# Performance work log

Hardware: AMD Instinct MI355X
Metric: run time of the kernel (lower is better)

## Reference

```python
import jax, jax.numpy as jnp
import numpy as np

N = 20000      # nodes
E = 320000     # edges (before self-loops)
D = 128        # esm_embeds
H = 4          # n_heads (layer 1)
G = 256        # graphs in batch
SLOPE = 0.2    # GATConv default negative_slope


def setup_inputs() -> dict:
    key = jax.random.key(0)
    ks = jax.random.split(key, 16)
    x = jax.random.normal(ks[0], (N, D), jnp.float32)
    src = jax.random.randint(ks[1], (E,), 0, N)
    off = jax.random.randint(ks[2], (E,), 1, N)
    dst = (src + off) % N  # guaranteed no self-loops (PyG removes then re-adds them)
    edge_index = jnp.stack([src, dst]).astype(jnp.int64)
    batch = jnp.sort(jax.random.randint(ks[3], (N,), 0, G)).astype(jnp.int64)
    s = 0.05
    W1 = jax.random.normal(ks[4], (D, H * D), jnp.float32) * s
    a_src1 = jax.random.normal(ks[5], (1, H, D), jnp.float32) * s
    a_dst1 = jax.random.normal(ks[6], (1, H, D), jnp.float32) * s
    b1 = jnp.zeros((H * D,), jnp.float32)
    W2 = jax.random.normal(ks[7], (H * D, D), jnp.float32) * s
    a_src2 = jax.random.normal(ks[8], (1, 1, D), jnp.float32) * s
    a_dst2 = jax.random.normal(ks[9], (1, 1, D), jnp.float32) * s
    b2 = jnp.zeros((D,), jnp.float32)
    fc1_w = jax.random.normal(ks[10], (D, 16), jnp.float32) * s
    fc1_b = jnp.zeros((16,), jnp.float32)
    fc2_w = jax.random.normal(ks[11], (16, 1), jnp.float32) * s
    fc2_b = jnp.zeros((1,), jnp.float32)
    return {"x": x, "edge_index": edge_index, "batch": batch,
            "W1": W1, "a_src1": a_src1, "a_dst1": a_dst1, "b1": b1,
            "W2": W2, "a_src2": a_src2, "a_dst2": a_dst2, "b2": b2,
            "fc1_w": fc1_w, "fc1_b": fc1_b, "fc2_w": fc2_w, "fc2_b": fc2_b}


def _gat_conv(h, src, dst, a_src, a_dst, n):
    """h: [n, heads, C]; returns aggregated [n, heads, C] (PyG GATConv message passing)."""
    al_s = jnp.sum(h * a_src, axis=-1)  # [n, heads]
    al_d = jnp.sum(h * a_dst, axis=-1)  # [n, heads]
    e = jax.nn.leaky_relu(al_s[src] + al_d[dst], SLOPE)  # [Etot, heads]
    m = jax.lax.stop_gradient(jax.ops.segment_max(e, dst, num_segments=n))
    ex = jnp.exp(e - m[dst])
    denom = jax.ops.segment_sum(ex, dst, num_segments=n)
    alpha = ex / denom[dst]                               # per-destination softmax
    msg = h[src] * alpha[..., None]                       # [Etot, heads, C]
    return jax.ops.segment_sum(msg, dst, num_segments=n)


def reference(x, edge_index, batch, W1, a_src1, a_dst1, b1,
              W2, a_src2, a_dst2, b2, fc1_w, fc1_b, fc2_w, fc2_b):
    n = x.shape[0]
    loop = jnp.arange(n, dtype=edge_index.dtype)
    src = jnp.concatenate([edge_index[0], loop])  # GATConv add_self_loops=True
    dst = jnp.concatenate([edge_index[1], loop])
    # layer 1: heads=H, concat -> [n, H*D], then ELU (dropout is identity in eval)
    h1 = (x @ W1).reshape(n, H, D)
    o1 = _gat_conv(h1, src, dst, a_src1, a_dst1, n).reshape(n, H * D) + b1
    x1 = jax.nn.elu(o1)
    # layer 2: heads=1, concat -> [n, D], then ReLU
    h2 = (x1 @ W2).reshape(n, 1, D)
    o2 = _gat_conv(h2, src, dst, a_src2, a_dst2, n).reshape(n, D) + b2
    x2 = jax.nn.relu(o2)
    # global max pool over graphs; x2 >= 0 so clamping handles any empty segment
    pooled = jnp.maximum(jax.ops.segment_max(x2, batch, num_segments=G), 0.0)
    hfc = jax.nn.relu(pooled @ fc1_w + fc1_b)
    return hfc @ fc2_w + fc2_b  # [G, 1]
```

## Files before the change

kernel.cpp:

```cpp
#include <hip/hip_runtime.h>
#include <hip/hip_fp16.h>

#define N_NODES 20000
#define E_EDGES 320000
#define D_DIM   128
#define H1HEADS 4
#define G_GRAPHS 256
#define SLOPE   0.2f

typedef _Float16 h8 __attribute__((ext_vector_type(8)));
typedef float float4v __attribute__((ext_vector_type(4)));

__global__ void cntprep_k(const int* __restrict__ dst, int* __restrict__ cnt,
                          const float* __restrict__ W1, __half* __restrict__ w1t,
                          const float* __restrict__ W2, __half* __restrict__ w2t) {
    int i = blockIdx.x * blockDim.x + threadIdx.x;
    if (i < E_EDGES) atomicAdd(&cnt[dst[i]], 1);
    if (i < 128 * 512) {
        {
            int k = i >> 9, n = i & 511;
            w1t[n * 128 + k] = __float2half(W1[i]);
        }
        {
            int k = i >> 7, n = i & 127;
            w2t[n * 512 + k] = __float2half(W2[i]);
        }
    }
}

#define SCAN_B 79
__global__ __launch_bounds__(256) void scan1_k(const int* __restrict__ cnt,
                                               int* __restrict__ part) {
    __shared__ int s[256];
    int t = threadIdx.x;
    int i = blockIdx.x * 256 + t;
    int v = (i < N_NODES) ? cnt[i] : 0;
    s[t] = v;
    __syncthreads();
    for (int off = 128; off > 0; off >>= 1) {
        if (t < off) s[t] += s[t + off];
        __syncthreads();
    }
    if (t == 0) part[blockIdx.x] = s[0];
}
__global__ __launch_bounds__(128) void scan2_k(int* __restrict__ part) {
    __shared__ int s[128];
    int t = threadIdx.x;
    int v = (t < SCAN_B) ? part[t] : 0;
    s[t] = v;
    __syncthreads();
    for (int off = 1; off < 128; off <<= 1) {
        int u = (t >= off) ? s[t - off] : 0;
        __syncthreads();
        s[t] += u;
        __syncthreads();
    }
    if (t < SCAN_B) part[t] = s[t] - v;
}
__global__ __launch_bounds__(256) void scan3_k(const int* __restrict__ cnt,
                                               const int* __restrict__ part,
                                               int* __restrict__ rowptr) {
    __shared__ int s[256];
    int t = threadIdx.x;
    int i = blockIdx.x * 256 + t;
    int v = (i < N_NODES) ? cnt[i] : 0;
    s[t] = v;
    __syncthreads();
    for (int off = 1; off < 256; off <<= 1) {
        int u = (t >= off) ? s[t - off] : 0;
        __syncthreads();
        s[t] += u;
        __syncthreads();
    }
    if (i < N_NODES) rowptr[i] = part[blockIdx.x] + s[t] - v;
    if (blockIdx.x == 0 && t == 0) rowptr[N_NODES] = E_EDGES;
}

__global__ void scat_k(const int* __restrict__ src, const int* __restrict__ dst,
                       const int* __restrict__ rowptr, int* __restrict__ cur,
                       int* __restrict__ csrsrc) {
    int e = blockIdx.x * blockDim.x + threadIdx.x;
    if (e >= E_EDGES) return;
    int d = dst[e];
    int p = rowptr[d] + atomicAdd(&cur[d], 1);
    csrsrc[p] = src[e];
}

__device__ __forceinline__ int bitonic64(int key, int lane) {
#pragma unroll
    for (int k = 2; k <= 64; k <<= 1) {
#pragma unroll
        for (int j = k >> 1; j > 0; j >>= 1) {
            int other = __shfl_xor(key, j);
            bool up = ((lane & k) == 0);
            bool lower = ((lane & j) == 0);
            int mn = min(key, other), mx = max(key, other);
            key = (up == lower) ? mn : mx;
        }
    }
    return key;
}

__global__ __launch_bounds__(256) void sortb_k(const int* __restrict__ rowptr,
                                               int* __restrict__ csrsrc) {
    const int node = (blockIdx.x * blockDim.x + threadIdx.x) >> 6;
    if (node >= N_NODES) return;
    const int lane = threadIdx.x & 63;
    const int r0 = rowptr[node];
    const int deg = rowptr[node + 1] - r0;
    if (deg <= 1 || deg > 64) return;
    int key = 0x7FFFFFFF;
    if (lane < deg) key = csrsrc[r0 + lane];
    key = bitonic64(key, lane);
    if (lane < deg) csrsrc[r0 + lane] = key;
}

__device__ __forceinline__ void store_val(__half* p, float v) { *p = __float2half(v); }
__device__ __forceinline__ void store_val(float* p, float v) { *p = v; }

template <typename OT>
__global__ __launch_bounds__(256) void fgemm_k(const float* __restrict__ A,
                                               const __half* __restrict__ BT,
                                               const int M, const int N, const int K,
                                               OT* __restrict__ C,
                                               float* __restrict__ als,
                                               float* __restrict__ ald,
                                               const float* __restrict__ asrc,
                                               const float* __restrict__ adst) {
    constexpr int SA = 72;
    __shared__ __half Ah[64 * SA], Al[64 * SA];
    __shared__ float sdot[64][2][2];
    const int t = threadIdx.x;
    const int wave = t >> 6, lane = t & 63;
    const int q = lane >> 4, rr = lane & 15;
    const int row0 = blockIdx.x * 64;
    const int col0 = blockIdx.y * 128;
    const int wm = wave & 1, wn = wave >> 1;
    const int H = gridDim.y;

    float4v acc[2][4];
#pragma unroll
    for (int i = 0; i < 2; ++i)
#pragma unroll
        for (int j = 0; j < 4; ++j) acc[i][j] = (float4v){0.f, 0.f, 0.f, 0.f};

    for (int kc = 0; kc < K; kc += 64) {
        __syncthreads();
#pragma unroll
        for (int i = 0; i < 4; ++i) {
            int u = t + i * 256;
            int m = u >> 4, mac = u & 15;
            int r = row0 + m;
            float4 fv = make_float4(0.f, 0.f, 0.f, 0.f);
            if (r < M) fv = *(const float4*)(A + (size_t)r * K + kc + mac * 4);
            union { __half h[4]; uint2 u2; } ph, pl;
            float f[4] = {fv.x, fv.y, fv.z, fv.w};
#pragma unroll
            for (int k = 0; k < 4; ++k) {
                __half hb = __float2half(f[k]);
                ph.h[k] = hb;
                pl.h[k] = __float2half(f[k] - __half2float(hb));
            }
            *(uint2*)(Ah + m * SA + mac * 4) = ph.u2;
            *(uint2*)(Al + m * SA + mac * 4) = pl.u2;
        }
        __syncthreads();
#pragma unroll
        for (int ks = 0; ks < 2; ++ks) {
            const int ko = ks * 32 + q * 8;
            h8 ah[2], alo[2], bh[4];
#pragma unroll
            for (int mt = 0; mt < 2; ++mt) {
                int m = (wm * 2 + mt) * 16 + rr;
                ah[mt]  = *(const h8*)(Ah + m * SA + ko);
                alo[mt] = *(const h8*)(Al + m * SA + ko);
            }
#pragma unroll
            for (int nt = 0; nt < 4; ++nt) {
                int n = (wn * 4 + nt) * 16 + rr;
                bh[nt] = *(const h8*)(BT + (size_t)(col0 + n) * K + kc + ko);
            }
#pragma unroll
            for (int mt = 0; mt < 2; ++mt)
#pragma unroll
                for (int nt = 0; nt < 4; ++nt) {
                    acc[mt][nt] = __builtin_amdgcn_mfma_f32_16x16x32_f16(
                        ah[mt], bh[nt], acc[mt][nt], 0, 0, 0);
                    acc[mt][nt] = __builtin_amdgcn_mfma_f32_16x16x32_f16(
                        alo[mt], bh[nt], acc[mt][nt], 0, 0, 0);
                }
        }
    }
#pragma unroll
    for (int mt = 0; mt < 2; ++mt) {
#pragma unroll
        for (int reg = 0; reg < 4; ++reg) {
            int r = row0 + (wm * 2 + mt) * 16 + q * 4 + reg;
            if (r < M) {
#pragma unroll
                for (int nt = 0; nt < 4; ++nt) {
                    int c = col0 + (wn * 4 + nt) * 16 + rr;
                    store_val(&C[(size_t)r * N + c], acc[mt][nt][reg]);
                }
            }
        }
    }
    ((float*)sdot)[t] = 0.f;
    __syncthreads();
    const float* as = asrc + blockIdx.y * 128;
    const float* ad = adst + blockIdx.y * 128;
#pragma unroll
    for (int mt = 0; mt < 2; ++mt) {
#pragma unroll
        for (int reg = 0; reg < 4; ++reg) {
            float ps = 0.f, pd = 0.f;
#pragma unroll
            for (int nt = 0; nt < 4; ++nt) {
                int cc = (wn * 4 + nt) * 16 + rr;
                float v = acc[mt][nt][reg];
                ps += v * as[cc];
                pd += v * ad[cc];
            }
#pragma unroll
            for (int off = 1; off < 16; off <<= 1) {
                ps += __shfl_xor(ps, off);
                pd += __shfl_xor(pd, off);
            }
            if (rr == 0) {
                int row = (wm * 2 + mt) * 16 + q * 4 + reg;
                sdot[row][wn][0] = ps;
                sdot[row][wn][1] = pd;
            }
        }
    }
    __syncthreads();
    if (t < 64) {
        int r = row0 + t;
        if (r < M) {
            als[r * H + blockIdx.y] = sdot[t][0][0] + sdot[t][1][0];
            ald[r * H + blockIdx.y] = sdot[t][0][1] + sdot[t][1][1];
        }
    }
}

__device__ __forceinline__ float lrelu(float v) { return (v > 0.f) ? v : SLOPE * v; }

__global__ __launch_bounds__(64) void agg1_k(const __half* __restrict__ h,
                                             const float4* __restrict__ als4,
                                             const float4* __restrict__ ald4,
                                             const int* __restrict__ rowptr,
                                             const int* __restrict__ csrsrc,
                                             const float* __restrict__ bias,
                                             float* __restrict__ x1) {
    __shared__ int   ss[64];
    __shared__ float ws[64][4];
    const int node = blockIdx.x;
    const int lane = threadIdx.x;
    const int head = lane >> 4;
    const int r0 = rowptr[node];
    const int deg = rowptr[node + 1] - r0;
    const int tot = deg + 1;
    const float4 aldn = ald4[node];

    float acc[8] = {};
    float4 d4;

    if (tot <= 64) {
        int s = node;
        if (lane < deg) s = csrsrc[r0 + lane];
        float4 l4 = make_float4(-1e30f, -1e30f, -1e30f, -1e30f);
        if (lane < tot) {
            float4 a = als4[s];
            l4.x = lrelu(a.x + aldn.x); l4.y = lrelu(a.y + aldn.y);
            l4.z = lrelu(a.z + aldn.z); l4.w = lrelu(a.w + aldn.w);
        }
        float4 m4 = l4;
#pragma unroll
        for (int off = 32; off > 0; off >>= 1) {
            m4.x = fmaxf(m4.x, __shfl_xor(m4.x, off));
            m4.y = fmaxf(m4.y, __shfl_xor(m4.y, off));
            m4.z = fmaxf(m4.z, __shfl_xor(m4.z, off));
            m4.w = fmaxf(m4.w, __shfl_xor(m4.w, off));
        }
        float4 w4 = make_float4(0.f, 0.f, 0.f, 0.f);
        if (lane < tot) {
            w4.x = expf(l4.x - m4.x); w4.y = expf(l4.y - m4.y);
            w4.z = expf(l4.z - m4.z); w4.w = expf(l4.w - m4.w);
        }
        d4 = w4;
#pragma unroll
        for (int off = 32; off > 0; off >>= 1) {
            d4.x += __shfl_xor(d4.x, off);
            d4.y += __shfl_xor(d4.y, off);
            d4.z += __shfl_xor(d4.z, off);
            d4.w += __shfl_xor(d4.w, off);
        }
        ss[lane] = s;
        *(float4*)&ws[lane][0] = w4;
        const uint4* hp = (const uint4*)h;
        int j = 0;
        for (; j + 8 <= tot; j += 8) {
            uint4 k0 = hp[(size_t)ss[j]     * 64 + lane];
            uint4 k1 = hp[(size_t)ss[j + 1] * 64 + lane];
            uint4 k2 = hp[(size_t)ss[j + 2] * 64 + lane];
            uint4 k3 = hp[(size_t)ss[j + 3] * 64 + lane];
            uint4 k4 = hp[(size_t)ss[j + 4] * 64 + lane];
            uint4 k5 = hp[(size_t)ss[j + 5] * 64 + lane];
            uint4 k6 = hp[(size_t)ss[j + 6] * 64 + lane];
            uint4 k7 = hp[(size_t)ss[j + 7] * 64 + lane];
            float w0 = ws[j][head],     w1 = ws[j + 1][head];
            float w2 = ws[j + 2][head], w3 = ws[j + 3][head];
            float w4s = ws[j + 4][head], w5 = ws[j + 5][head];
            float w6 = ws[j + 6][head], w7 = ws[j + 7][head];
            const __half *p0 = (const __half*)&k0, *p1 = (const __half*)&k1;
            const __half *p2 = (const __half*)&k2, *p3 = (const __half*)&k3;
            const __half *p4 = (const __half*)&k4, *p5 = (const __half*)&k5;
            const __half *p6 = (const __half*)&k6, *p7 = (const __half*)&k7;
#pragma unroll
            for (int k = 0; k < 8; ++k) acc[k] += w0 * __half2float(p0[k]);
#pragma unroll
            for (int k = 0; k < 8; ++k) acc[k] += w1 * __half2float(p1[k]);
#pragma unroll
            for (int k = 0; k < 8; ++k) acc[k] += w2 * __half2float(p2[k]);
#pragma unroll
            for (int k = 0; k < 8; ++k) acc[k] += w3 * __half2float(p3[k]);
#pragma unroll
            for (int k = 0; k < 8; ++k) acc[k] += w4s * __half2float(p4[k]);
#pragma unroll
            for (int k = 0; k < 8; ++k) acc[k] += w5 * __half2float(p5[k]);
#pragma unroll
            for (int k = 0; k < 8; ++k) acc[k] += w6 * __half2float(p6[k]);
#pragma unroll
            for (int k = 0; k < 8; ++k) acc[k] += w7 * __half2float(p7[k]);
        }
        for (; j + 4 <= tot; j += 4) {
            uint4 k0 = hp[(size_t)ss[j]     * 64 + lane];
            uint4 k1 = hp[(size_t)ss[j + 1] * 64 + lane];
            uint4 k2 = hp[(size_t)ss[j + 2] * 64 + lane];
            uint4 k3 = hp[(size_t)ss[j + 3] * 64 + lane];
            float w0 = ws[j][head],     w1 = ws[j + 1][head];
            float w2 = ws[j + 2][head], w3 = ws[j + 3][head];
            const __half *p0 = (const __half*)&k0, *p1 = (const __half*)&k1;
            const __half *p2 = (const __half*)&k2, *p3 = (const __half*)&k3;
#pragma unroll
            for (int k = 0; k < 8; ++k) acc[k] += w0 * __half2float(p0[k]);
#pragma unroll
            for (int k = 0; k < 8; ++k) acc[k] += w1 * __half2float(p1[k]);
#pragma unroll
            for (int k = 0; k < 8; ++k) acc[k] += w2 * __half2float(p2[k]);
#pragma unroll
            for (int k = 0; k < 8; ++k) acc[k] += w3 * __half2float(p3[k]);
        }
        for (; j < tot; ++j) {
            uint4 pk = hp[(size_t)ss[j] * 64 + lane];
            float wj = ws[j][head];
            const __half* p = (const __half*)&pk;
#pragma unroll
            for (int k = 0; k < 8; ++k) acc[k] += wj * __half2float(p[k]);
        }
    } else {
        float4 m4 = make_float4(-1e30f, -1e30f, -1e30f, -1e30f);
        for (int base = 0; base < tot; base += 64) {
            int j = base + lane;
            float4 l4 = make_float4(-1e30f, -1e30f, -1e30f, -1e30f);
            if (j < tot) {
                int s = (j < deg) ? csrsrc[r0 + j] : node;
                float4 a = als4[s];
                l4.x = lrelu(a.x + aldn.x); l4.y = lrelu(a.y + aldn.y);
                l4.z = lrelu(a.z + aldn.z); l4.w = lrelu(a.w + aldn.w);
            }
#pragma unroll
            for (int off = 32; off > 0; off >>= 1) {
                l4.x = fmaxf(l4.x, __shfl_xor(l4.x, off));
                l4.y = fmaxf(l4.y, __shfl_xor(l4.y, off));
                l4.z = fmaxf(l4.z, __shfl_xor(l4.z, off));
                l4.w = fmaxf(l4.w, __shfl_xor(l4.w, off));
            }
            m4.x = fmaxf(m4.x, l4.x); m4.y = fmaxf(m4.y, l4.y);
            m4.z = fmaxf(m4.z, l4.z); m4.w = fmaxf(m4.w, l4.w);
        }
        d4 = make_float4(0.f, 0.f, 0.f, 0.f);
        for (int base = 0; base < tot; base += 64) {
            int j = base + lane;
            int s = node;
            float4 w4 = make_float4(0.f, 0.f, 0.f, 0.f);
            if (j < tot) {
                if (j < deg) s = csrsrc[r0 + j];
                float4 a = als4[s];
                w4.x = expf(lrelu(a.x + aldn.x) - m4.x);
                w4.y = expf(lrelu(a.y + aldn.y) - m4.y);
                w4.z = expf(lrelu(a.z + aldn.z) - m4.z);
                w4.w = expf(lrelu(a.w + aldn.w) - m4.w);
            }
            float4 p4 = w4;
#pragma unroll
            for (int off = 32; off > 0; off >>= 1) {
                p4.x += __shfl_xor(p4.x, off);
                p4.y += __shfl_xor(p4.y, off);
                p4.z += __shfl_xor(p4.z, off);
                p4.w += __shfl_xor(p4.w, off);
            }
            d4.x += p4.x; d4.y += p4.y; d4.z += p4.z; d4.w += p4.w;
            int lim = min(64, tot - base);
            for (int j2 = 0; j2 < lim; ++j2) {
                int sj = __shfl(s, j2);
                float w0 = __shfl(w4.x, j2), w1 = __shfl(w4.y, j2);
                float w2 = __shfl(w4.z, j2), w3 = __shfl(w4.w, j2);
                float wj = (head < 2) ? (head == 0 ? w0 : w1) : (head == 2 ? w2 : w3);
                const uint4 pk = *((const uint4*)(h + (size_t)sj * 512) + lane);
                const __half* p = (const __half*)&pk;
#pragma unroll
                for (int k = 0; k < 8; ++k) acc[k] += wj * __half2float(p[k]);
            }
        }
    }

    const float dsel = (head < 2) ? (head == 0 ? d4.x : d4.y) : (head == 2 ? d4.z : d4.w);
    const float inv = 1.f / dsel;
    const float4 b0 = ((const float4*)bias)[lane * 2];
    const float4 b1 = ((const float4*)bias)[lane * 2 + 1];
    float v[8];
    v[0] = acc[0] * inv + b0.x; v[1] = acc[1] * inv + b0.y;
    v[2] = acc[2] * inv + b0.z; v[3] = acc[3] * inv + b0.w;
    v[4] = acc[4] * inv + b1.x; v[5] = acc[5] * inv + b1.y;
    v[6] = acc[6] * inv + b1.z; v[7] = acc[7] * inv + b1.w;
#pragma unroll
    for (int k = 0; k < 8; ++k) v[k] = (v[k] > 0.f) ? v[k] : expm1f(v[k]);
    float4* orow = (float4*)(x1 + (size_t)node * 512);
    orow[lane * 2]     = make_float4(v[0], v[1], v[2], v[3]);
    orow[lane * 2 + 1] = make_float4(v[4], v[5], v[6], v[7]);
}

__global__ __launch_bounds__(64) void agg2_k(const __half* __restrict__ h,
                                             const float* __restrict__ als,
                                             const float* __restrict__ ald,
                                             const int* __restrict__ rowptr,
                                             const int* __restrict__ csrsrc,
                                             const float* __restrict__ bias,
                                             const int* __restrict__ batch,
                                             int* __restrict__ pooled) {
    __shared__ int   ss[64];
    __shared__ float ws[64];
    const int node = blockIdx.x;
    const int lane = threadIdx.x;
    const int r0 = rowptr[node];
    const int deg = rowptr[node + 1] - r0;
    const int tot = deg + 1;
    const float aldn = ald[node];

    float acc0 = 0.f, acc1 = 0.f;
    float denom;

    if (tot <= 64) {
        int s = node;
        if (lane < deg) s = csrsrc[r0 + lane];
        float l = -1e30f, w = 0.f;
        if (lane < tot) l = lrelu(als[s] + aldn);
        float m = l;
#pragma unroll
        for (int off = 32; off > 0; off >>= 1) m = fmaxf(m, __shfl_xor(m, off));
        if (lane < tot) w = expf(l - m);
        denom = w;
#pragma unroll
        for (int off = 32; off > 0; off >>= 1) denom += __shfl_xor(denom, off);
        ss[lane] = s;
        ws[lane] = w;
        const unsigned* hp = (const unsigned*)h;
        int j = 0;
        for (; j + 8 <= tot; j += 8) {
            unsigned k0 = hp[(size_t)ss[j]     * 64 + lane];
            unsigned k1 = hp[(size_t)ss[j + 1] * 64 + lane];
            unsigned k2 = hp[(size_t)ss[j + 2] * 64 + lane];
            unsigned k3 = hp[(size_t)ss[j + 3] * 64 + lane];
            unsigned k4 = hp[(size_t)ss[j + 4] * 64 + lane];
            unsigned k5 = hp[(size_t)ss[j + 5] * 64 + lane];
            unsigned k6 = hp[(size_t)ss[j + 6] * 64 + lane];
            unsigned k7 = hp[(size_t)ss[j + 7] * 64 + lane];
            float w0 = ws[j], w1 = ws[j + 1], w2 = ws[j + 2], w3 = ws[j + 3];
            float w4 = ws[j + 4], w5 = ws[j + 5], w6 = ws[j + 6], w7 = ws[j + 7];
            float2 f0 = __half22float2(*(__half2*)&k0);
            float2 f1 = __half22float2(*(__half2*)&k1);
            float2 f2 = __half22float2(*(__half2*)&k2);
            float2 f3 = __half22float2(*(__half2*)&k3);
            float2 f4 = __half22float2(*(__half2*)&k4);
            float2 f5 = __half22float2(*(__half2*)&k5);
            float2 f6 = __half22float2(*(__half2*)&k6);
            float2 f7 = __half22float2(*(__half2*)&k7);
            acc0 += w0 * f0.x; acc1 += w0 * f0.y;
            acc0 += w1 * f1.x; acc1 += w1 * f1.y;
            acc0 += w2 * f2.x; acc1 += w2 * f2.y;
            acc0 += w3 * f3.x; acc1 += w3 * f3.y;
            acc0 += w4 * f4.x; acc1 += w4 * f4.y;
            acc0 += w5 * f5.x; acc1 += w5 * f5.y;
            acc0 += w6 * f6.x; acc1 += w6 * f6.y;
            acc0 += w7 * f7.x; acc1 += w7 * f7.y;
        }
        for (; j < tot; ++j) {
            unsigned pk = hp[(size_t)ss[j] * 64 + lane];
            float wj = ws[j];
            float2 f = __half22float2(*(__half2*)&pk);
            acc0 += wj * f.x;
            acc1 += wj * f.y;
        }
    } else {
        float m = -1e30f;
        for (int base = 0; base < tot; base += 64) {
            int j = base + lane;
            float l = -1e30f;
            if (j < tot) {
                int s = (j < deg) ? csrsrc[r0 + j] : node;
                l = lrelu(als[s] + aldn);
            }
#pragma unroll
            for (int off = 32; off > 0; off >>= 1) l = fmaxf(l, __shfl_xor(l, off));
            m = fmaxf(m, l);
        }
        denom = 0.f;
        for (int base = 0; base < tot; base += 64) {
            int j = base + lane;
            int s = node;
            float w = 0.f;
            if (j < tot) {
                if (j < deg) s = csrsrc[r0 + j];
                w = expf(lrelu(als[s] + aldn) - m);
            }
            float ws2 = w;
#pragma unroll
            for (int off = 32; off > 0; off >>= 1) ws2 += __shfl_xor(ws2, off);
            denom += ws2;
            int lim = min(64, tot - base);
            for (int j2 = 0; j2 < lim; ++j2) {
                int sj = __shfl(s, j2);
                float wj = __shfl(w, j2);
                float2 f = __half22float2(((const __half2*)(h + (size_t)sj * 128))[lane]);
                acc0 += wj * f.x;
                acc1 += wj * f.y;
            }
        }
    }

    const float inv = 1.f / denom;
    float v0 = fmaxf(acc0 * inv + bias[lane * 2], 0.f);
    float v1 = fmaxf(acc1 * inv + bias[lane * 2 + 1], 0.f);
    int* pb = pooled + batch[node] * 128;
    atomicMax(&pb[lane * 2], __float_as_int(v0));
    atomicMax(&pb[lane * 2 + 1], __float_as_int(v1));
}

__global__ __launch_bounds__(64) void fc_k(const float* __restrict__ pooled,
                                           const float* __restrict__ w1,
                                           const float* __restrict__ b1,
                                           const float* __restrict__ w2,
                                           const float* __restrict__ b2,
                                           float* __restrict__ out) {
    int g = blockIdx.x;
    __shared__ float p[128];
    int t = threadIdx.x;
    p[t] = pooled[g * 128 + t];
    p[t + 64] = pooled[g * 128 + 64 + t];
    __syncthreads();
    float acc = 0.f;
    if (t < 16) {
        float s = b1[t];
        for (int c = 0; c < 128; ++c) s += p[c] * w1[c * 16 + t];
        s = fmaxf(s, 0.f);
        acc = s * w2[t];
    }
#pragma unroll
    for (int off = 8; off > 0; off >>= 1) acc += __shfl_down(acc, off);
    if (t == 0) out[g] = acc + b2[0];
}

extern "C" void kernel_launch(void* const* d_in, const int* in_sizes, int n_in,
                              void* d_out, int out_size, void* d_ws, size_t ws_size,
                              hipStream_t stream) {
    const float* x      = (const float*)d_in[0];
    const int*   ei     = (const int*)d_in[1];
    const int*   batch  = (const int*)d_in[2];
    const float* W1     = (const float*)d_in[3];
    const float* a_src1 = (const float*)d_in[4];
    const float* a_dst1 = (const float*)d_in[5];
    const float* b1     = (const float*)d_in[6];
    const float* W2     = (const float*)d_in[7];
    const float* a_src2 = (const float*)d_in[8];
    const float* a_dst2 = (const float*)d_in[9];
    const float* b2     = (const float*)d_in[10];
    const float* fc1w   = (const float*)d_in[11];
    const float* fc1b   = (const float*)d_in[12];
    const float* fc2w   = (const float*)d_in[13];
    const float* fc2b   = (const float*)d_in[14];
    float* out = (float*)d_out;

    const int* src = ei;
    const int* dst = ei + E_EDGES;

    int*   cnt    = (int*)d_ws;
    int*   cur    = cnt + 20000;
    int*   pooled = cur + 20000;
    int*   rowptr = pooled + 32768;
    int*   part   = rowptr + 20004;
    int*   csrsrc = part + 128;
    __half* h1h   = (__half*)(csrsrc + 320000);
    __half* h2h   = h1h + 10240000;
    float* als1   = (float*)(h2h + 2560000);
    float* ald1   = als1 + 80000;
    float* als2   = ald1 + 80000;
    float* ald2   = als2 + 20000;
    __half* w1t   = (__half*)(ald2 + 20000);
    __half* w2t   = w1t + 65536;
    float* x1     = (float*)(w2t + 65536);

    (void)hipMemsetAsync(d_ws, 0, 72768 * 4, stream);

    cntprep_k<<<(E_EDGES + 255) / 256, 256, 0, stream>>>(dst, cnt, W1, w1t, W2, w2t);
    scan1_k<<<SCAN_B, 256, 0, stream>>>(cnt, part);
    scan2_k<<<1, 128, 0, stream>>>(part);
    scan3_k<<<SCAN_B, 256, 0, stream>>>(cnt, part, rowptr);
    scat_k<<<(E_EDGES + 255) / 256, 256, 0, stream>>>(src, dst, rowptr, cur, csrsrc);
    sortb_k<<<N_NODES / 4, 256, 0, stream>>>(rowptr, csrsrc);

    fgemm_k<__half><<<dim3(313, 4), 256, 0, stream>>>(x, w1t, N_NODES, 512, 128, h1h,
                                                      als1, ald1, a_src1, a_dst1);

    agg1_k<<<N_NODES, 64, 0, stream>>>(h1h, (const float4*)als1, (const float4*)ald1,
                                       rowptr, csrsrc, b1, x1);

    fgemm_k<__half><<<dim3(313, 1), 256, 0, stream>>>(x1, w2t, N_NODES, 128, 512, h2h,
                                                      als2, ald2, a_src2, a_dst2);

    agg2_k<<<N_NODES, 64, 0, stream>>>(h2h, als2, ald2, rowptr, csrsrc, b2,
                                       batch, pooled);

    fc_k<<<G_GRAPHS, 64, 0, stream>>>((const float*)pooled, fc1w, fc1b, fc2w, fc2b, out);
}
```

Before: 275.5 us.

## Merge scan kernels, fold neighbor sort into aggregation, pack four nodes per block

```diff
diff --git a/kernel.cpp b/kernel.cpp
--- a/kernel.cpp
+++ b/kernel.cpp
@@ -28,52 +28,31 @@
     }
 }
 
-#define SCAN_B 79
-__global__ __launch_bounds__(256) void scan1_k(const int* __restrict__ cnt,
-                                               int* __restrict__ part) {
+__global__ __launch_bounds__(256) void scan_k(const int* __restrict__ cnt,
+                                              int* __restrict__ rowptr) {
     __shared__ int s[256];
-    int t = threadIdx.x;
-    int i = blockIdx.x * 256 + t;
-    int v = (i < N_NODES) ? cnt[i] : 0;
-    s[t] = v;
-    __syncthreads();
-    for (int off = 128; off > 0; off >>= 1) {
-        if (t < off) s[t] += s[t + off];
-        __syncthreads();
-    }
-    if (t == 0) part[blockIdx.x] = s[0];
-}
-__global__ __launch_bounds__(128) void scan2_k(int* __restrict__ part) {
-    __shared__ int s[128];
-    int t = threadIdx.x;
-    int v = (t < SCAN_B) ? part[t] : 0;
-    s[t] = v;
-    __syncthreads();
-    for (int off = 1; off < 128; off <<= 1) {
-        int u = (t >= off) ? s[t - off] : 0;
-        __syncthreads();
-        s[t] += u;
-        __syncthreads();
-    }
-    if (t < SCAN_B) part[t] = s[t] - v;
-}
-__global__ __launch_bounds__(256) void scan3_k(const int* __restrict__ cnt,
-                                               const int* __restrict__ part,
-                                               int* __restrict__ rowptr) {
-    __shared__ int s[256];
-    int t = threadIdx.x;
-    int i = blockIdx.x * 256 + t;
-    int v = (i < N_NODES) ? cnt[i] : 0;
-    s[t] = v;
+    const int t = threadIdx.x;
+    const int CH = (N_NODES + 255) / 256;
+    int base = t * CH;
+    int sum = 0;
+    for (int i = 0; i < CH; ++i) {
+        int idx = base + i;
+        if (idx < N_NODES) sum += cnt[idx];
+    }
+    s[t] = sum;
     __syncthreads();
     for (int off = 1; off < 256; off <<= 1) {
-        int u = (t >= off) ? s[t - off] : 0;
+        int v = (t >= off) ? s[t - off] : 0;
         __syncthreads();
-        s[t] += u;
+        s[t] += v;
         __syncthreads();
     }
-    if (i < N_NODES) rowptr[i] = part[blockIdx.x] + s[t] - v;
-    if (blockIdx.x == 0 && t == 0) rowptr[N_NODES] = E_EDGES;
+    int run = (t > 0) ? s[t - 1] : 0;
+    for (int i = 0; i < CH; ++i) {
+        int idx = base + i;
+        if (idx < N_NODES) { rowptr[idx] = run; run += cnt[idx]; }
+    }
+    if (t == 255) rowptr[N_NODES] = E_EDGES;
 }
 
 __global__ void scat_k(const int* __restrict__ src, const int* __restrict__ dst,
@@ -99,20 +78,6 @@
         }
     }
     return key;
-}
-
-__global__ __launch_bounds__(256) void sortb_k(const int* __restrict__ rowptr,
-                                               int* __restrict__ csrsrc) {
-    const int node = (blockIdx.x * blockDim.x + threadIdx.x) >> 6;
-    if (node >= N_NODES) return;
-    const int lane = threadIdx.x & 63;
-    const int r0 = rowptr[node];
-    const int deg = rowptr[node + 1] - r0;
-    if (deg <= 1 || deg > 64) return;
-    int key = 0x7FFFFFFF;
-    if (lane < deg) key = csrsrc[r0 + lane];
-    key = bitonic64(key, lane);
-    if (lane < deg) csrsrc[r0 + lane] = key;
 }
 
 __device__ __forceinline__ void store_val(__half* p, float v) { *p = __float2half(v); }
@@ -245,17 +210,19 @@
 
 __device__ __forceinline__ float lrelu(float v) { return (v > 0.f) ? v : SLOPE * v; }
 
-__global__ __launch_bounds__(64) void agg1_k(const __half* __restrict__ h,
-                                             const float4* __restrict__ als4,
-                                             const float4* __restrict__ ald4,
-                                             const int* __restrict__ rowptr,
-                                             const int* __restrict__ csrsrc,
-                                             const float* __restrict__ bias,
-                                             float* __restrict__ x1) {
-    __shared__ int   ss[64];
-    __shared__ float ws[64][4];
-    const int node = blockIdx.x;
-    const int lane = threadIdx.x;
+__global__ __launch_bounds__(256) void agg1_k(const __half* __restrict__ h,
+                                              const float4* __restrict__ als4,
+                                              const float4* __restrict__ ald4,
+                                              const int* __restrict__ rowptr,
+                                              const int* __restrict__ csrsrc,
+                                              const float* __restrict__ bias,
+                                              float* __restrict__ x1) {
+    __shared__ int   ss[4][64];
+    __shared__ float ws[4][64][4];
+    const int node = (blockIdx.x * blockDim.x + threadIdx.x) >> 6;
+    if (node >= N_NODES) return;
+    const int lane = threadIdx.x & 63;
+    const int wv = threadIdx.x >> 6;
     const int head = lane >> 4;
     const int r0 = rowptr[node];
     const int deg = rowptr[node + 1] - r0;
@@ -266,8 +233,11 @@
     float4 d4;
 
     if (tot <= 64) {
-        int s = node;
-        if (lane < deg) s = csrsrc[r0 + lane];
+        int key = 0x7FFFFFFF;
+        if (lane < deg) key = csrsrc[r0 + lane];
+        else if (lane == deg) key = node;
+        key = bitonic64(key, lane);
+        int s = (lane < tot) ? key : node;
         float4 l4 = make_float4(-1e30f, -1e30f, -1e30f, -1e30f);
         if (lane < tot) {
             float4 a = als4[s];
@@ -295,23 +265,23 @@
             d4.z += __shfl_xor(d4.z, off);
             d4.w += __shfl_xor(d4.w, off);
         }
-        ss[lane] = s;
-        *(float4*)&ws[lane][0] = w4;
+        ss[wv][lane] = s;
+        *(float4*)&ws[wv][lane][0] = w4;
         const uint4* hp = (const uint4*)h;
         int j = 0;
         for (; j + 8 <= tot; j += 8) {
-            uint4 k0 = hp[(size_t)ss[j]     * 64 + lane];
-            uint4 k1 = hp[(size_t)ss[j + 1] * 64 + lane];
-            uint4 k2 = hp[(size_t)ss[j + 2] * 64 + lane];
-            uint4 k3 = hp[(size_t)ss[j + 3] * 64 + lane];
-            uint4 k4 = hp[(size_t)ss[j + 4] * 64 + lane];
-            uint4 k5 = hp[(size_t)ss[j + 5] * 64 + lane];
-            uint4 k6 = hp[(size_t)ss[j + 6] * 64 + lane];
-            uint4 k7 = hp[(size_t)ss[j + 7] * 64 + lane];
-            float w0 = ws[j][head],     w1 = ws[j + 1][head];
-            float w2 = ws[j + 2][head], w3 = ws[j + 3][head];
-            float w4s = ws[j + 4][head], w5 = ws[j + 5][head];
-            float w6 = ws[j + 6][head], w7 = ws[j + 7][head];
+            uint4 k0 = hp[(size_t)ss[wv][j]     * 64 + lane];
+            uint4 k1 = hp[(size_t)ss[wv][j + 1] * 64 + lane];
+            uint4 k2 = hp[(size_t)ss[wv][j + 2] * 64 + lane];
+            uint4 k3 = hp[(size_t)ss[wv][j + 3] * 64 + lane];
+            uint4 k4 = hp[(size_t)ss[wv][j + 4] * 64 + lane];
+            uint4 k5 = hp[(size_t)ss[wv][j + 5] * 64 + lane];
+            uint4 k6 = hp[(size_t)ss[wv][j + 6] * 64 + lane];
+            uint4 k7 = hp[(size_t)ss[wv][j + 7] * 64 + lane];
+            float w0 = ws[wv][j][head],     w1 = ws[wv][j + 1][head];
+            float w2 = ws[wv][j + 2][head], w3 = ws[wv][j + 3][head];
+            float w4s = ws[wv][j + 4][head], w5 = ws[wv][j + 5][head];
+            float w6 = ws[wv][j + 6][head], w7 = ws[wv][j + 7][head];
             const __half *p0 = (const __half*)&k0, *p1 = (const __half*)&k1;
             const __half *p2 = (const __half*)&k2, *p3 = (const __half*)&k3;
             const __half *p4 = (const __half*)&k4, *p5 = (const __half*)&k5;
@@ -334,12 +304,12 @@
             for (int k = 0; k < 8; ++k) acc[k] += w7 * __half2float(p7[k]);
         }
         for (; j + 4 <= tot; j += 4) {
-            uint4 k0 = hp[(size_t)ss[j]     * 64 + lane];
-            uint4 k1 = hp[(size_t)ss[j + 1] * 64 + lane];
-            uint4 k2 = hp[(size_t)ss[j + 2] * 64 + lane];
-            uint4 k3 = hp[(size_t)ss[j + 3] * 64 + lane];
-            float w0 = ws[j][head],     w1 = ws[j + 1][head];
-            float w2 = ws[j + 2][head], w3 = ws[j + 3][head];
+            uint4 k0 = hp[(size_t)ss[wv][j]     * 64 + lane];
+            uint4 k1 = hp[(size_t)ss[wv][j + 1] * 64 + lane];
+            uint4 k2 = hp[(size_t)ss[wv][j + 2] * 64 + lane];
+            uint4 k3 = hp[(size_t)ss[wv][j + 3] * 64 + lane];
+            float w0 = ws[wv][j][head],     w1 = ws[wv][j + 1][head];
+            float w2 = ws[wv][j + 2][head], w3 = ws[wv][j + 3][head];
             const __half *p0 = (const __half*)&k0, *p1 = (const __half*)&k1;
             const __half *p2 = (const __half*)&k2, *p3 = (const __half*)&k3;
 #pragma unroll
@@ -352,8 +322,8 @@
             for (int k = 0; k < 8; ++k) acc[k] += w3 * __half2float(p3[k]);
         }
         for (; j < tot; ++j) {
-            uint4 pk = hp[(size_t)ss[j] * 64 + lane];
-            float wj = ws[j][head];
+            uint4 pk = hp[(size_t)ss[wv][j] * 64 + lane];
+            float wj = ws[wv][j][head];
             const __half* p = (const __half*)&pk;
 #pragma unroll
             for (int k = 0; k < 8; ++k) acc[k] += wj * __half2float(p[k]);
@@ -431,18 +401,20 @@
     orow[lane * 2 + 1] = make_float4(v[4], v[5], v[6], v[7]);
 }
 
-__global__ __launch_bounds__(64) void agg2_k(const __half* __restrict__ h,
-                                             const float* __restrict__ als,
-                                             const float* __restrict__ ald,
-                                             const int* __restrict__ rowptr,
-                                             const int* __restrict__ csrsrc,
-                                             const float* __restrict__ bias,
-                                             const int* __restrict__ batch,
-                                             int* __restrict__ pooled) {
-    __shared__ int   ss[64];
-    __shared__ float ws[64];
-    const int node = blockIdx.x;
-    const int lane = threadIdx.x;
+__global__ __launch_bounds__(256) void agg2_k(const __half* __restrict__ h,
+                                              const float* __restrict__ als,
+                                              const float* __restrict__ ald,
+                                              const int* __restrict__ rowptr,
+                                              const int* __restrict__ csrsrc,
+                                              const float* __restrict__ bias,
+                                              const int* __restrict__ batch,
+                                              int* __restrict__ pooled) {
+    __shared__ int   ss[4][64];
+    __shared__ float ws[4][64];
+    const int node = (blockIdx.x * blockDim.x + threadIdx.x) >> 6;
+    if (node >= N_NODES) return;
+    const int lane = threadIdx.x & 63;
+    const int wv = threadIdx.x >> 6;
     const int r0 = rowptr[node];
     const int deg = rowptr[node + 1] - r0;
     const int tot = deg + 1;
@@ -452,8 +424,11 @@
     float denom;
 
     if (tot <= 64) {
-        int s = node;
-        if (lane < deg) s = csrsrc[r0 + lane];
+        int key = 0x7FFFFFFF;
+        if (lane < deg) key = csrsrc[r0 + lane];
+        else if (lane == deg) key = node;
+        key = bitonic64(key, lane);
+        int s = (lane < tot) ? key : node;
         float l = -1e30f, w = 0.f;
         if (lane < tot) l = lrelu(als[s] + aldn);
         float m = l;
@@ -463,21 +438,23 @@
         denom = w;
 #pragma unroll
         for (int off = 32; off > 0; off >>= 1) denom += __shfl_xor(denom, off);
-        ss[lane] = s;
-        ws[lane] = w;
+        ss[wv][lane] = s;
+        ws[wv][lane] = w;
         const unsigned* hp = (const unsigned*)h;
         int j = 0;
         for (; j + 8 <= tot; j += 8) {
-            unsigned k0 = hp[(size_t)ss[j]     * 64 + lane];
-            unsigned k1 = hp[(size_t)ss[j + 1] * 64 + lane];
-            unsigned k2 = hp[(size_t)ss[j + 2] * 64 + lane];
-            unsigned k3 = hp[(size_t)ss[j + 3] * 64 + lane];
-            unsigned k4 = hp[(size_t)ss[j + 4] * 64 + lane];
-            unsigned k5 = hp[(size_t)ss[j + 5] * 64 + lane];
-            unsigned k6 = hp[(size_t)ss[j + 6] * 64 + lane];
-            unsigned k7 = hp[(size_t)ss[j + 7] * 64 + lane];
-            float w0 = ws[j], w1 = ws[j + 1], w2 = ws[j + 2], w3 = ws[j + 3];
-            float w4 = ws[j + 4], w5 = ws[j + 5], w6 = ws[j + 6], w7 = ws[j + 7];
+            unsigned k0 = hp[(size_t)ss[wv][j]     * 64 + lane];
+            unsigned k1 = hp[(size_t)ss[wv][j + 1] * 64 + lane];
+            unsigned k2 = hp[(size_t)ss[wv][j + 2] * 64 + lane];
+            unsigned k3 = hp[(size_t)ss[wv][j + 3] * 64 + lane];
+            unsigned k4 = hp[(size_t)ss[wv][j + 4] * 64 + lane];
+            unsigned k5 = hp[(size_t)ss[wv][j + 5] * 64 + lane];
+            unsigned k6 = hp[(size_t)ss[wv][j + 6] * 64 + lane];
+            unsigned k7 = hp[(size_t)ss[wv][j + 7] * 64 + lane];
+            float w0 = ws[wv][j], w1 = ws[wv][j + 1];
+            float w2 = ws[wv][j + 2], w3 = ws[wv][j + 3];
+            float w4 = ws[wv][j + 4], w5 = ws[wv][j + 5];
+            float w6 = ws[wv][j + 6], w7 = ws[wv][j + 7];
             float2 f0 = __half22float2(*(__half2*)&k0);
             float2 f1 = __half22float2(*(__half2*)&k1);
             float2 f2 = __half22float2(*(__half2*)&k2);
@@ -496,8 +473,8 @@
             acc0 += w7 * f7.x; acc1 += w7 * f7.y;
         }
         for (; j < tot; ++j) {
-            unsigned pk = hp[(size_t)ss[j] * 64 + lane];
-            float wj = ws[j];
+            unsigned pk = hp[(size_t)ss[wv][j] * 64 + lane];
+            float wj = ws[wv][j];
             float2 f = __half22float2(*(__half2*)&pk);
             acc0 += wj * f.x;
             acc1 += wj * f.y;
@@ -598,8 +575,7 @@
     int*   cur    = cnt + 20000;
     int*   pooled = cur + 20000;
     int*   rowptr = pooled + 32768;
-    int*   part   = rowptr + 20004;
-    int*   csrsrc = part + 128;
+    int*   csrsrc = rowptr + 20004;
     __half* h1h   = (__half*)(csrsrc + 320000);
     __half* h2h   = h1h + 10240000;
     float* als1   = (float*)(h2h + 2560000);
@@ -613,23 +589,20 @@
     (void)hipMemsetAsync(d_ws, 0, 72768 * 4, stream);
 
     cntprep_k<<<(E_EDGES + 255) / 256, 256, 0, stream>>>(dst, cnt, W1, w1t, W2, w2t);
-    scan1_k<<<SCAN_B, 256, 0, stream>>>(cnt, part);
-    scan2_k<<<1, 128, 0, stream>>>(part);
-    scan3_k<<<SCAN_B, 256, 0, stream>>>(cnt, part, rowptr);
+    scan_k<<<1, 256, 0, stream>>>(cnt, rowptr);
     scat_k<<<(E_EDGES + 255) / 256, 256, 0, stream>>>(src, dst, rowptr, cur, csrsrc);
-    sortb_k<<<N_NODES / 4, 256, 0, stream>>>(rowptr, csrsrc);
 
     fgemm_k<__half><<<dim3(313, 4), 256, 0, stream>>>(x, w1t, N_NODES, 512, 128, h1h,
                                                       als1, ald1, a_src1, a_dst1);
 
-    agg1_k<<<N_NODES, 64, 0, stream>>>(h1h, (const float4*)als1, (const float4*)ald1,
-                                       rowptr, csrsrc, b1, x1);
+    agg1_k<<<N_NODES / 4, 256, 0, stream>>>(h1h, (const float4*)als1, (const float4*)ald1,
+                                            rowptr, csrsrc, b1, x1);
 
     fgemm_k<__half><<<dim3(313, 1), 256, 0, stream>>>(x1, w2t, N_NODES, 128, 512, h2h,
                                                       als2, ald2, a_src2, a_dst2);
 
-    agg2_k<<<N_NODES, 64, 0, stream>>>(h2h, als2, ald2, rowptr, csrsrc, b2,
-                                       batch, pooled);
+    agg2_k<<<N_NODES / 4, 256, 0, stream>>>(h2h, als2, ald2, rowptr, csrsrc, b2,
+                                            batch, pooled);
 
     fc_k<<<G_GRAPHS, 64, 0, stream>>>((const float*)pooled, fc1w, fc1b, fc2w, fc2b, out);
 }
```

Result: slower. 310.7 us (+12.8%).
